# Performance work log

Hardware: AMD Instinct MI355X
Metric: run time of the kernel (lower is better)

## Reference

```python
import jax, jax.numpy as jnp
import numpy as np

STRIDE = 1
PAD = 1
K = 3
BN_EPS = 1e-5


def conv2d(x, w, b, stride, padding):
    out = jax.lax.conv_general_dilated(
        x, w, (stride, stride), [(padding, padding), (padding, padding)],
        dimension_numbers=("NCHW", "OIHW", "NCHW"))
    return out + b[None, :, None, None]


def _bilinear_gather(xb, sy, sx):
    # Zero-fill outside bounds (torchvision DeformConv2d semantics).
    Hin, Win = xb.shape[1], xb.shape[2]
    y0 = jnp.floor(sy)
    x0 = jnp.floor(sx)
    y1 = y0 + 1.0
    x1 = x0 + 1.0
    wy1 = sy - y0
    wy0 = 1.0 - wy1
    wx1 = sx - x0
    wx0 = 1.0 - wx1

    def g(yi, xi):
        valid = (yi >= 0) & (yi < Hin) & (xi >= 0) & (xi < Win)
        yc = jnp.clip(yi, 0, Hin - 1).astype(jnp.int32)
        xc = jnp.clip(xi, 0, Win - 1).astype(jnp.int32)
        v = xb[:, yc, xc]  # [C, K2, Hout, Wout]
        return v * valid[None].astype(xb.dtype)

    return (g(y0, x0) * (wy0 * wx0)[None] + g(y0, x1) * (wy0 * wx1)[None]
            + g(y1, x0) * (wy1 * wx0)[None] + g(y1, x1) * (wy1 * wx1)[None])


def deform_conv2d(x, offset, w, b, stride, padding):
    B, C, Hin, Win = x.shape
    O = w.shape[0]
    K2 = K * K
    Hout, Wout = offset.shape[2], offset.shape[3]
    # torchvision layout: channel 2*k = dy, 2*k+1 = dx, k row-major over kernel
    off = offset.reshape(B, K2, 2, Hout, Wout)
    dy, dx = off[:, :, 0], off[:, :, 1]
    ki, kj = jnp.meshgrid(jnp.arange(K), jnp.arange(K), indexing="ij")
    ki = ki.reshape(K2).astype(x.dtype)
    kj = kj.reshape(K2).astype(x.dtype)
    oy = (jnp.arange(Hout) * stride - padding).astype(x.dtype)
    ox = (jnp.arange(Wout) * stride - padding).astype(x.dtype)
    sy = ki[None, :, None, None] + oy[None, None, :, None] + dy  # [B,K2,Hout,Wout]
    sx = kj[None, :, None, None] + ox[None, None, None, :] + dx
    sampled = jax.vmap(_bilinear_gather)(x, sy, sx)  # [B, C, K2, Hout, Wout]
    out = jnp.einsum("bckhw,ock->bohw", sampled, w.reshape(O, C, K2))
    return out + b[None, :, None, None]


def batchnorm_train(x, gamma, beta):
    # training-mode BN: biased batch stats over (N, H, W)
    mean = jnp.mean(x, axis=(0, 2, 3), keepdims=True)
    var = jnp.mean(jnp.square(x - mean), axis=(0, 2, 3), keepdims=True)
    xn = (x - mean) * jax.lax.rsqrt(var + BN_EPS)
    return xn * gamma[None, :, None, None] + beta[None, :, None, None]


def setup_inputs() -> dict:
    key = jax.random.key(0)
    ks = jax.random.split(key, 4)
    B, C, H, W = 8, 64, 128, 128
    O = 64
    x = jax.random.normal(ks[0], (B, C, H, W), dtype=jnp.float32)
    fan_off = C * K * K
    offset_w = jax.random.normal(ks[1], (2 * K * K, C, K, K), dtype=jnp.float32) / np.sqrt(fan_off)
    offset_b = jnp.zeros((2 * K * K,), dtype=jnp.float32)
    deform_w = jax.random.normal(ks[2], (O, C, K, K), dtype=jnp.float32) / np.sqrt(fan_off)
    deform_b = jnp.zeros((O,), dtype=jnp.float32)
    bn_gamma = jnp.ones((O,), dtype=jnp.float32)
    bn_beta = jnp.zeros((O,), dtype=jnp.float32)
    prelu_a = jnp.full((1,), 0.2, dtype=jnp.float32)
    return {"x": x, "offset_w": offset_w, "offset_b": offset_b,
            "deform_w": deform_w, "deform_b": deform_b,
            "bn_gamma": bn_gamma, "bn_beta": bn_beta, "prelu_a": prelu_a}


def reference(x, offset_w, offset_b, deform_w, deform_b, bn_gamma, bn_beta, prelu_a):
    offset = conv2d(x, offset_w, offset_b, STRIDE, PAD)
    y = deform_conv2d(x, offset, deform_w, deform_b, STRIDE, PAD)
    y = batchnorm_train(y, bn_gamma, bn_beta)
    return jnp.where(y >= 0, y, prelu_a[0] * y)
```

## Files before the change

### kernel.cpp

```cpp
#include <hip/hip_runtime.h>
#include <hip/hip_bf16.h>
#include <hip/hip_fp16.h>

typedef float f32x4 __attribute__((ext_vector_type(4)));
typedef unsigned int u32;
typedef u32 u32x4 __attribute__((ext_vector_type(4)));
typedef __bf16 bf16x8 __attribute__((ext_vector_type(8)));
typedef short s16x8 __attribute__((ext_vector_type(8)));
typedef unsigned short u16;

#define HWSZ 16384
#define NPIX 131072

#define XT_OFF    0u
#define YB_OFF    16777216u
#define PART_OFF  33554432u
#define WB_OFF    42991616u
#define STATS_OFF 43106816u
#define WO_OFF    43107840u

__device__ inline u32 pkbf(float lo, float hi) {
  u16 l = __builtin_bit_cast(u16, __float2bfloat16(lo));
  u16 h = __builtin_bit_cast(u16, __float2bfloat16(hi));
  return (u32)l | ((u32)h << 16);
}
__device__ inline float bflo(u32 u) { return __builtin_bit_cast(float, u << 16); }
__device__ inline float bfhi(u32 u) { return __builtin_bit_cast(float, u & 0xFFFF0000u); }

__global__ void kprep(const float* __restrict__ dw, const float* __restrict__ ow,
                      u16* __restrict__ Wb, u16* __restrict__ Wo) {
  int t = blockIdx.x * 256 + threadIdx.x;
  if (t < 36864) {
    int o = t / 576, r = t % 576;
    int c = r / 9, k2 = r % 9;
    __hip_bfloat16 h = __float2bfloat16(dw[t]);
    Wb[o * 576 + k2 * 64 + c] = __builtin_bit_cast(u16, h);
  } else if (t < 55296) {
    int t2 = t - 36864;
    int oc = t2 / 576, r = t2 % 576;
    int c = r / 9, k2 = r % 9;
    float v = (oc < 18) ? ow[(oc * 64 + c) * 9 + k2] : 0.f;
    __hip_bfloat16 h = __float2bfloat16(v);
    Wo[oc * 576 + k2 * 64 + c] = __builtin_bit_cast(u16, h);
  }
}

__global__ void ktrans(const float* __restrict__ x, u16* __restrict__ xt) {
  __shared__ float tile[64][65];
  int blk = blockIdx.x;
  int b = blk >> 8, hwT = (blk & 255) * 64;
  int tid = threadIdx.x;
  int tx = tid & 63, ty = tid >> 6;
  const float* xp = x + (size_t)b * 64 * HWSZ;
#pragma unroll
  for (int r = 0; r < 16; ++r) {
    int c = r * 4 + ty;
    tile[c][tx] = xp[c * HWSZ + hwT + tx];
  }
  __syncthreads();
  u16* xo = xt + ((size_t)b * HWSZ + hwT) * 64;
  int o8 = (tid & 7) * 8;
#pragma unroll
  for (int r = 0; r < 2; ++r) {
    int hwl = r * 32 + (tid >> 3);
    u32x4 out;
#pragma unroll
    for (int j = 0; j < 4; ++j)
      out[j] = pkbf(tile[o8 + 2 * j][hwl], tile[o8 + 2 * j + 1][hwl]);
    *(u32x4*)&xo[(size_t)hwl * 64 + o8] = out;
  }
}

__global__ __launch_bounds__(256, 4) void kmain(
    const u16* __restrict__ xt, const u16* __restrict__ Wo,
    const float* __restrict__ offb, const u16* __restrict__ Wb,
    const float* __restrict__ db, u16* __restrict__ yb,
    float* __restrict__ part) {
  __shared__ u16 S2[2][128 * 64];
  __shared__ u32 mWp[1152 * 2];
  __shared__ u32 mPos[1152];
  float* OFFT = (float*)&S2[0][0];
  int tid = threadIdx.x;
  int lane = tid & 63, wid = tid >> 6;
  int bid = blockIdx.x;
  int batch = bid & 7, tilei = bid >> 3;
  int base = (batch << 14) + tilei * 128;
  int b = batch;
  int h0 = tilei;

  int oct = lane & 7;
  int p0 = wid * 8 + (lane >> 3);
  int oct16 = oct << 4, oct8 = oct << 3;
  int q8 = (lane >> 4) * 8;
  const char* xb = (const char*)xt;

  int ocb2 = wid & 1, pxb4 = (wid >> 1) * 4;
  int orow_o = ocb2 * 16 + (lane & 15);
  f32x4 acco[4];
#pragma unroll
  for (int t2 = 0; t2 < 4; ++t2) acco[t2] = {0.f, 0.f, 0.f, 0.f};
#pragma unroll
  for (int k = 0; k < 9; ++k) {
#pragma unroll
    for (int pi = 0; pi < 4; ++pi) {
      int pp = p0 + pi * 32;
      int yy = h0 - 1 + k / 3, xx = pp - 1 + k % 3;
      bool v = ((unsigned)yy < 128u) && ((unsigned)xx < 128u);
      const char* pb =
          v ? xb + (size_t)(((b << 14) + yy * 128 + xx) * 128) + oct16 : xb;
      u32x4 g = *(const u32x4*)pb;
      u32 msk = v ? 0xFFFFFFFFu : 0u;
      u32x4 out;
#pragma unroll
      for (int j = 0; j < 4; ++j) out[j] = g[j] & msk;
      *(u32x4*)&S2[k & 1][(pp * 64 + oct8) ^ ((pp & 7) << 3)] = out;
    }
    __syncthreads();
#pragma unroll
    for (int h = 0; h < 2; ++h) {
      int kc = 2 * k + h;
      s16x8 a = *(const s16x8*)(Wo + orow_o * 576 + kc * 32 + q8);
#pragma unroll
      for (int t2 = 0; t2 < 4; ++t2) {
        int row = (pxb4 + t2) * 16 + (lane & 15);
        int idx = (row * 64 + h * 32 + q8) ^ ((row & 7) << 3);
        bf16x8 bb = __builtin_bit_cast(bf16x8, *(const s16x8*)&S2[k & 1][idx]);
        acco[t2] = __builtin_amdgcn_mfma_f32_16x16x32_bf16(
            __builtin_bit_cast(bf16x8, a), bb, acco[t2], 0, 0, 0);
      }
    }
  }
  __syncthreads();

#pragma unroll
  for (int t2 = 0; t2 < 4; ++t2) {
    int pixl = (pxb4 + t2) * 16 + (lane & 15);
    int ocb = ocb2 * 16 + (lane >> 4) * 4;
#pragma unroll
    for (int r = 0; r < 4; ++r) {
      int oc = ocb + r;
      if (oc < 18) OFFT[pixl * 20 + oc] = acco[t2][r] + offb[oc];
    }
  }
  __syncthreads();

  for (int t = tid; t < 1152; t += 256) {
    int tp = t / 9, k2 = t - tp * 9;
    int pix = base + tp;
    int hw = pix & 16383;
    int hh = hw >> 7, ww = hw & 127;
    float dy = OFFT[tp * 20 + 2 * k2];
    float dx = OFFT[tp * 20 + 2 * k2 + 1];
    float sy = (float)(hh - 1 + k2 / 3) + dy;
    float sx = (float)(ww - 1 + k2 % 3) + dx;
    float fy = floorf(sy), fx = floorf(sx);
    int y0 = (int)fy, x0 = (int)fx;
    float wy1 = sy - fy, wx1 = sx - fx;
    float ay0 = ((unsigned)y0 < 128u) ? 1.f - wy1 : 0.f;
    float ay1 = ((unsigned)(y0 + 1) < 128u) ? wy1 : 0.f;
    float ax0 = ((unsigned)x0 < 128u) ? 1.f - wx1 : 0.f;
    float ax1 = ((unsigned)(x0 + 1) < 128u) ? wx1 : 0.f;
    int y0c = min(max(y0, 0), 127), x0c = min(max(x0, 0), 127);
    int dys = min(max(y0 + 1, 0), 127) - y0c;
    int dxs = min(max(x0 + 1, 0), 127) - x0c;
    mWp[t * 2]     = __builtin_bit_cast(u32, __floats2half2_rn(ay0 * ax0, ay0 * ax1));
    mWp[t * 2 + 1] = __builtin_bit_cast(u32, __floats2half2_rn(ay1 * ax0, ay1 * ax1));
    mPos[t] = (u32)(((b << 14) + y0c * 128 + x0c) * 128) | (u32)dxs | ((u32)dys << 1);
  }
  __syncthreads();

  f32x4 acc[8];
#pragma unroll
  for (int nb = 0; nb < 8; ++nb) acc[nb] = {0.f, 0.f, 0.f, 0.f};
  int orow_d = wid * 16 + (lane & 15);
#pragma unroll
  for (int k = 0; k < 9; ++k) {
#pragma unroll
    for (int pi = 0; pi < 4; ++pi) {
      int pp = p0 + pi * 32;
      int t = pp * 9 + k;
      u32 wlo = mWp[t * 2], whi = mWp[t * 2 + 1];
      u32 pm = mPos[t];
      u32 dxB = (pm & 1u) << 7;
      u32 dyB = (pm & 2u) << 13;
      const char* pb = xb + (pm & 0xFFFFFF80u) + oct16;
      u32x4 c00 = *(const u32x4*)pb;
      u32x4 c01 = *(const u32x4*)(pb + dxB);
      u32x4 c10 = *(const u32x4*)(pb + dyB);
      u32x4 c11 = *(const u32x4*)(pb + dyB + dxB);
      __half2 hl = __builtin_bit_cast(__half2, wlo);
      __half2 hh2 = __builtin_bit_cast(__half2, whi);
      float w00 = __low2float(hl), w01 = __high2float(hl);
      float w10 = __low2float(hh2), w11 = __high2float(hh2);
      u32x4 out;
#pragma unroll
      for (int j = 0; j < 4; ++j) {
        float sL = fmaf(w11, bflo(c11[j]), fmaf(w10, bflo(c10[j]),
                   fmaf(w01, bflo(c01[j]), w00 * bflo(c00[j]))));
        float sH = fmaf(w11, bfhi(c11[j]), fmaf(w10, bfhi(c10[j]),
                   fmaf(w01, bfhi(c01[j]), w00 * bfhi(c00[j]))));
        out[j] = pkbf(sL, sH);
      }
      *(u32x4*)&S2[k & 1][(pp * 64 + oct8) ^ ((pp & 7) << 3)] = out;
    }
    __syncthreads();
#pragma unroll
    for (int h = 0; h < 2; ++h) {
      int kc = 2 * k + h;
      s16x8 a = *(const s16x8*)(Wb + orow_d * 576 + kc * 32 + q8);
#pragma unroll
      for (int nb = 0; nb < 8; ++nb) {
        int row = nb * 16 + (lane & 15);
        int idx = (row * 64 + h * 32 + q8) ^ ((row & 7) << 3);
        bf16x8 bb = __builtin_bit_cast(bf16x8, *(const s16x8*)&S2[k & 1][idx]);
        acc[nb] = __builtin_amdgcn_mfma_f32_16x16x32_bf16(
            __builtin_bit_cast(bf16x8, a), bb, acc[nb], 0, 0, 0);
      }
    }
  }

  int obase = wid * 16 + (lane >> 4) * 4;
  float s1[4] = {0, 0, 0, 0}, s2[4] = {0, 0, 0, 0};
#pragma unroll
  for (int nb = 0; nb < 8; ++nb) {
    int pix = base + nb * 16 + (lane & 15);
    int hw = pix & 16383;
    u16* yp = yb + (size_t)b * (64 * HWSZ) + hw;
#pragma unroll
    for (int r = 0; r < 4; ++r) {
      int o = obase + r;
      float v = acc[nb][r] + db[o];
      yp[(size_t)o * HWSZ] = __builtin_bit_cast(u16, __float2bfloat16(v));
      s1[r] += v;
      s2[r] += v * v;
    }
  }
#pragma unroll
  for (int m = 1; m < 16; m <<= 1) {
#pragma unroll
    for (int r = 0; r < 4; ++r) {
      s1[r] += __shfl_xor(s1[r], m, 64);
      s2[r] += __shfl_xor(s2[r], m, 64);
    }
  }
  if ((lane & 15) == 0) {
    float* pp = part + (size_t)bid * 128;
#pragma unroll
    for (int r = 0; r < 4; ++r) {
      pp[obase + r] = s1[r];
      pp[64 + obase + r] = s2[r];
    }
  }
}

__global__ void kbnf(const float* __restrict__ part, const float* __restrict__ gamma,
                     const float* __restrict__ beta, float* __restrict__ stats) {
  __shared__ float r1[256], r2[256];
  int o = blockIdx.x;
  int tid = threadIdx.x;
  float s1 = 0.f, s2 = 0.f;
  for (int i = tid; i < 1024; i += 256) {
    s1 += part[(size_t)i * 128 + o];
    s2 += part[(size_t)i * 128 + 64 + o];
  }
  r1[tid] = s1; r2[tid] = s2;
  __syncthreads();
  for (int s = 128; s > 0; s >>= 1) {
    if (tid < s) { r1[tid] += r1[tid + s]; r2[tid] += r2[tid + s]; }
    __syncthreads();
  }
  if (tid == 0) {
    float m = r1[0] * (1.f / 131072.f);
    float v = r2[0] * (1.f / 131072.f) - m * m;
    float sc = gamma[o] * rsqrtf(v + 1e-5f);
    stats[128 + o] = sc;
    stats[192 + o] = beta[o] - m * sc;
  }
}

__global__ void kfinal(const u16* __restrict__ yb, float* __restrict__ y,
                       const float* __restrict__ stats, const float* __restrict__ pa) {
  float a = pa[0];
  int total = NPIX * 64 / 8;
  for (int i = blockIdx.x * blockDim.x + threadIdx.x; i < total;
       i += gridDim.x * blockDim.x) {
    int o = (i >> 11) & 63;
    u32x4 v = ((const u32x4*)yb)[i];
    float sc = stats[128 + o], sh = stats[192 + o];
    f32x4 o0, o1;
#pragma unroll
    for (int j = 0; j < 4; ++j) {
      float tL = fmaf(bflo(v[j]), sc, sh);
      float tH = fmaf(bfhi(v[j]), sc, sh);
      float rL = tL >= 0.f ? tL : a * tL;
      float rH = tH >= 0.f ? tH : a * tH;
      if (j < 2) { o0[2 * j] = rL; o0[2 * j + 1] = rH; }
      else       { o1[2 * (j - 2)] = rL; o1[2 * (j - 2) + 1] = rH; }
    }
    ((f32x4*)y)[2 * i] = o0;
    ((f32x4*)y)[2 * i + 1] = o1;
  }
}

extern "C" void kernel_launch(void* const* d_in, const int* in_sizes, int n_in,
                              void* d_out, int out_size, void* d_ws, size_t ws_size,
                              hipStream_t stream) {
  const float* x  = (const float*)d_in[0];
  const float* ow = (const float*)d_in[1];
  const float* ob = (const float*)d_in[2];
  const float* dw = (const float*)d_in[3];
  const float* db = (const float*)d_in[4];
  const float* gm = (const float*)d_in[5];
  const float* bt = (const float*)d_in[6];
  const float* pa = (const float*)d_in[7];
  char* ws = (char*)d_ws;
  u16*   xt    = (u16*)(ws + XT_OFF);
  u16*   yb    = (u16*)(ws + YB_OFF);
  float* part  = (float*)(ws + PART_OFF);
  u16*   Wb    = (u16*)(ws + WB_OFF);
  u16*   Wo    = (u16*)(ws + WO_OFF);
  float* stats = (float*)(ws + STATS_OFF);
  float* y = (float*)d_out;

  kprep<<<216, 256, 0, stream>>>(dw, ow, Wb, Wo);
  ktrans<<<2048, 256, 0, stream>>>(x, xt);
  kmain<<<1024, 256, 0, stream>>>(xt, Wo, ob, Wb, db, yb, part);
  kbnf<<<64, 256, 0, stream>>>(part, gm, bt, stats);
  kfinal<<<2048, 256, 0, stream>>>(yb, y, stats, pa);
}
```

Before: 92.27 us.

## Halve pixel tile to 64 and process two kernel taps per barrier stage

The main fused kernel now handles 64 pixels per block instead of a full 128-pixel row, doubling the grid to 2048 blocks. The 9 kernel taps are grouped in pairs, so each barrier stage stages two taps into shared memory, cutting the number of __syncthreads from 9 to 5 per GEMM phase. The aim is more parallelism, fewer barriers and lower accumulator register pressure. The cost is less weight reuse per block, twice as many partial-stat rows for the BN reduction, and more redundant offset-conv loads at tile edges.

New measurement: 95.84 us. 3.9% more time.

```diff
diff --git a/kernel.cpp b/kernel.cpp
--- a/kernel.cpp
+++ b/kernel.cpp
@@ -76,17 +76,18 @@
     const float* __restrict__ offb, const u16* __restrict__ Wb,
     const float* __restrict__ db, u16* __restrict__ yb,
     float* __restrict__ part) {
-  __shared__ u16 S2[2][128 * 64];
-  __shared__ u32 mWp[1152 * 2];
-  __shared__ u32 mPos[1152];
-  float* OFFT = (float*)&S2[0][0];
+  __shared__ u16 S2[2][2][64 * 64];
+  __shared__ u32 mWp[576 * 2];
+  __shared__ u32 mPos[576];
+  float* OFFT = (float*)&S2[0][0][0];
   int tid = threadIdx.x;
   int lane = tid & 63, wid = tid >> 6;
   int bid = blockIdx.x;
   int batch = bid & 7, tilei = bid >> 3;
-  int base = (batch << 14) + tilei * 128;
+  int base = (batch << 14) + tilei * 64;
   int b = batch;
-  int h0 = tilei;
+  int hw0 = base & 16383;
+  int h0 = hw0 >> 7, w0 = hw0 & 127;
 
   int oct = lane & 7;
   int p0 = wid * 8 + (lane >> 3);
@@ -94,47 +95,60 @@
   int q8 = (lane >> 4) * 8;
   const char* xb = (const char*)xt;
 
-  int ocb2 = wid & 1, pxb4 = (wid >> 1) * 4;
+  int ocb2 = wid & 1, pxb2 = (wid >> 1) * 2;
   int orow_o = ocb2 * 16 + (lane & 15);
-  f32x4 acco[4];
-#pragma unroll
-  for (int t2 = 0; t2 < 4; ++t2) acco[t2] = {0.f, 0.f, 0.f, 0.f};
-#pragma unroll
-  for (int k = 0; k < 9; ++k) {
-#pragma unroll
-    for (int pi = 0; pi < 4; ++pi) {
-      int pp = p0 + pi * 32;
-      int yy = h0 - 1 + k / 3, xx = pp - 1 + k % 3;
-      bool v = ((unsigned)yy < 128u) && ((unsigned)xx < 128u);
-      const char* pb =
-          v ? xb + (size_t)(((b << 14) + yy * 128 + xx) * 128) + oct16 : xb;
-      u32x4 g = *(const u32x4*)pb;
-      u32 msk = v ? 0xFFFFFFFFu : 0u;
-      u32x4 out;
-#pragma unroll
-      for (int j = 0; j < 4; ++j) out[j] = g[j] & msk;
-      *(u32x4*)&S2[k & 1][(pp * 64 + oct8) ^ ((pp & 7) << 3)] = out;
+  f32x4 acco[2];
+  acco[0] = {0.f, 0.f, 0.f, 0.f};
+  acco[1] = {0.f, 0.f, 0.f, 0.f};
+#pragma unroll
+  for (int s = 0; s < 5; ++s) {
+    int ntap = (s < 4) ? 2 : 1;
+#pragma unroll
+    for (int ti = 0; ti < 2; ++ti) {
+      if (ti < ntap) {
+        int k = 2 * s + ti;
+#pragma unroll
+        for (int pi = 0; pi < 2; ++pi) {
+          int pp = p0 + pi * 32;
+          int yy = h0 - 1 + k / 3, xx = w0 + pp - 1 + k % 3;
+          bool v = ((unsigned)yy < 128u) && ((unsigned)xx < 128u);
+          const char* pb =
+              v ? xb + (size_t)(((b << 14) + yy * 128 + xx) * 128) + oct16 : xb;
+          u32x4 g = *(const u32x4*)pb;
+          u32 msk = v ? 0xFFFFFFFFu : 0u;
+          u32x4 out;
+#pragma unroll
+          for (int j = 0; j < 4; ++j) out[j] = g[j] & msk;
+          *(u32x4*)&S2[s & 1][ti][(pp * 64 + oct8) ^ ((pp & 7) << 3)] = out;
+        }
+      }
     }
     __syncthreads();
 #pragma unroll
-    for (int h = 0; h < 2; ++h) {
-      int kc = 2 * k + h;
-      s16x8 a = *(const s16x8*)(Wo + orow_o * 576 + kc * 32 + q8);
-#pragma unroll
-      for (int t2 = 0; t2 < 4; ++t2) {
-        int row = (pxb4 + t2) * 16 + (lane & 15);
-        int idx = (row * 64 + h * 32 + q8) ^ ((row & 7) << 3);
-        bf16x8 bb = __builtin_bit_cast(bf16x8, *(const s16x8*)&S2[k & 1][idx]);
-        acco[t2] = __builtin_amdgcn_mfma_f32_16x16x32_bf16(
-            __builtin_bit_cast(bf16x8, a), bb, acco[t2], 0, 0, 0);
+    for (int ti = 0; ti < 2; ++ti) {
+      if (ti < ntap) {
+#pragma unroll
+        for (int h = 0; h < 2; ++h) {
+          int kc = (2 * s + ti) * 2 + h;
+          s16x8 a = *(const s16x8*)(Wo + orow_o * 576 + kc * 32 + q8);
+#pragma unroll
+          for (int t2 = 0; t2 < 2; ++t2) {
+            int row = (pxb2 + t2) * 16 + (lane & 15);
+            int idx = (row * 64 + h * 32 + q8) ^ ((row & 7) << 3);
+            bf16x8 bb =
+                __builtin_bit_cast(bf16x8, *(const s16x8*)&S2[s & 1][ti][idx]);
+            acco[t2] = __builtin_amdgcn_mfma_f32_16x16x32_bf16(
+                __builtin_bit_cast(bf16x8, a), bb, acco[t2], 0, 0, 0);
+          }
+        }
       }
     }
   }
   __syncthreads();
 
 #pragma unroll
-  for (int t2 = 0; t2 < 4; ++t2) {
-    int pixl = (pxb4 + t2) * 16 + (lane & 15);
+  for (int t2 = 0; t2 < 2; ++t2) {
+    int pixl = (pxb2 + t2) * 16 + (lane & 15);
     int ocb = ocb2 * 16 + (lane >> 4) * 4;
 #pragma unroll
     for (int r = 0; r < 4; ++r) {
@@ -144,7 +158,7 @@
   }
   __syncthreads();
 
-  for (int t = tid; t < 1152; t += 256) {
+  for (int t = tid; t < 576; t += 256) {
     int tp = t / 9, k2 = t - tp * 9;
     int pix = base + tp;
     int hw = pix & 16383;
@@ -169,52 +183,65 @@
   }
   __syncthreads();
 
-  f32x4 acc[8];
-#pragma unroll
-  for (int nb = 0; nb < 8; ++nb) acc[nb] = {0.f, 0.f, 0.f, 0.f};
+  f32x4 acc[4];
+#pragma unroll
+  for (int nb = 0; nb < 4; ++nb) acc[nb] = {0.f, 0.f, 0.f, 0.f};
   int orow_d = wid * 16 + (lane & 15);
 #pragma unroll
-  for (int k = 0; k < 9; ++k) {
-#pragma unroll
-    for (int pi = 0; pi < 4; ++pi) {
-      int pp = p0 + pi * 32;
-      int t = pp * 9 + k;
-      u32 wlo = mWp[t * 2], whi = mWp[t * 2 + 1];
-      u32 pm = mPos[t];
-      u32 dxB = (pm & 1u) << 7;
-      u32 dyB = (pm & 2u) << 13;
-      const char* pb = xb + (pm & 0xFFFFFF80u) + oct16;
-      u32x4 c00 = *(const u32x4*)pb;
-      u32x4 c01 = *(const u32x4*)(pb + dxB);
-      u32x4 c10 = *(const u32x4*)(pb + dyB);
-      u32x4 c11 = *(const u32x4*)(pb + dyB + dxB);
-      __half2 hl = __builtin_bit_cast(__half2, wlo);
-      __half2 hh2 = __builtin_bit_cast(__half2, whi);
-      float w00 = __low2float(hl), w01 = __high2float(hl);
-      float w10 = __low2float(hh2), w11 = __high2float(hh2);
-      u32x4 out;
-#pragma unroll
-      for (int j = 0; j < 4; ++j) {
-        float sL = fmaf(w11, bflo(c11[j]), fmaf(w10, bflo(c10[j]),
-                   fmaf(w01, bflo(c01[j]), w00 * bflo(c00[j]))));
-        float sH = fmaf(w11, bfhi(c11[j]), fmaf(w10, bfhi(c10[j]),
-                   fmaf(w01, bfhi(c01[j]), w00 * bfhi(c00[j]))));
-        out[j] = pkbf(sL, sH);
+  for (int s = 0; s < 5; ++s) {
+    int ntap = (s < 4) ? 2 : 1;
+#pragma unroll
+    for (int ti = 0; ti < 2; ++ti) {
+      if (ti < ntap) {
+        int k = 2 * s + ti;
+#pragma unroll
+        for (int pi = 0; pi < 2; ++pi) {
+          int pp = p0 + pi * 32;
+          int t = pp * 9 + k;
+          u32 wlo = mWp[t * 2], whi = mWp[t * 2 + 1];
+          u32 pm = mPos[t];
+          u32 dxB = (pm & 1u) << 7;
+          u32 dyB = (pm & 2u) << 13;
+          const char* pb = xb + (pm & 0xFFFFFF80u) + oct16;
+          u32x4 c00 = *(const u32x4*)pb;
+          u32x4 c01 = *(const u32x4*)(pb + dxB);
+          u32x4 c10 = *(const u32x4*)(pb + dyB);
+          u32x4 c11 = *(const u32x4*)(pb + dyB + dxB);
+          __half2 hl = __builtin_bit_cast(__half2, wlo);
+          __half2 hh2 = __builtin_bit_cast(__half2, whi);
+          float w00 = __low2float(hl), w01 = __high2float(hl);
+          float w10 = __low2float(hh2), w11 = __high2float(hh2);
+          u32x4 out;
+#pragma unroll
+          for (int j = 0; j < 4; ++j) {
+            float sL = fmaf(w11, bflo(c11[j]), fmaf(w10, bflo(c10[j]),
+                       fmaf(w01, bflo(c01[j]), w00 * bflo(c00[j]))));
+            float sH = fmaf(w11, bfhi(c11[j]), fmaf(w10, bfhi(c10[j]),
+                       fmaf(w01, bfhi(c01[j]), w00 * bfhi(c00[j]))));
+            out[j] = pkbf(sL, sH);
+          }
+          *(u32x4*)&S2[s & 1][ti][(pp * 64 + oct8) ^ ((pp & 7) << 3)] = out;
+        }
       }
-      *(u32x4*)&S2[k & 1][(pp * 64 + oct8) ^ ((pp & 7) << 3)] = out;
     }
     __syncthreads();
 #pragma unroll
-    for (int h = 0; h < 2; ++h) {
-      int kc = 2 * k + h;
-      s16x8 a = *(const s16x8*)(Wb + orow_d * 576 + kc * 32 + q8);
-#pragma unroll
-      for (int nb = 0; nb < 8; ++nb) {
-        int row = nb * 16 + (lane & 15);
-        int idx = (row * 64 + h * 32 + q8) ^ ((row & 7) << 3);
-        bf16x8 bb = __builtin_bit_cast(bf16x8, *(const s16x8*)&S2[k & 1][idx]);
-        acc[nb] = __builtin_amdgcn_mfma_f32_16x16x32_bf16(
-            __builtin_bit_cast(bf16x8, a), bb, acc[nb], 0, 0, 0);
+    for (int ti = 0; ti < 2; ++ti) {
+      if (ti < ntap) {
+#pragma unroll
+        for (int h = 0; h < 2; ++h) {
+          int kc = (2 * s + ti) * 2 + h;
+          s16x8 a = *(const s16x8*)(Wb + orow_d * 576 + kc * 32 + q8);
+#pragma unroll
+          for (int nb = 0; nb < 4; ++nb) {
+            int row = nb * 16 + (lane & 15);
+            int idx = (row * 64 + h * 32 + q8) ^ ((row & 7) << 3);
+            bf16x8 bb =
+                __builtin_bit_cast(bf16x8, *(const s16x8*)&S2[s & 1][ti][idx]);
+            acc[nb] = __builtin_amdgcn_mfma_f32_16x16x32_bf16(
+                __builtin_bit_cast(bf16x8, a), bb, acc[nb], 0, 0, 0);
+          }
+        }
       }
     }
   }
@@ -222,7 +249,7 @@
   int obase = wid * 16 + (lane >> 4) * 4;
   float s1[4] = {0, 0, 0, 0}, s2[4] = {0, 0, 0, 0};
 #pragma unroll
-  for (int nb = 0; nb < 8; ++nb) {
+  for (int nb = 0; nb < 4; ++nb) {
     int pix = base + nb * 16 + (lane & 15);
     int hw = pix & 16383;
     u16* yp = yb + (size_t)b * (64 * HWSZ) + hw;
@@ -259,7 +286,7 @@
   int o = blockIdx.x;
   int tid = threadIdx.x;
   float s1 = 0.f, s2 = 0.f;
-  for (int i = tid; i < 1024; i += 256) {
+  for (int i = tid; i < 2048; i += 256) {
     s1 += part[(size_t)i * 128 + o];
     s2 += part[(size_t)i * 128 + 64 + o];
   }
@@ -324,7 +351,7 @@
 
   kprep<<<216, 256, 0, stream>>>(dw, ow, Wb, Wo);
   ktrans<<<2048, 256, 0, stream>>>(x, xt);
-  kmain<<<1024, 256, 0, stream>>>(xt, Wo, ob, Wb, db, yb, part);
+  kmain<<<2048, 256, 0, stream>>>(xt, Wo, ob, Wb, db, yb, part);
   kbnf<<<64, 256, 0, stream>>>(part, gm, bt, stats);
   kfinal<<<2048, 256, 0, stream>>>(yb, y, stats, pa);
 }
```
